# Optimization experiments

Hardware: AMD Instinct MI355X
Metric: run time of the kernel (lower is better)

Reference implementation:

```python
import jax, jax.numpy as jnp
import numpy as np

NHEADS = 16
KVHEADS = 4
HEAD_DIM = 128  # emb_kq_per_head == emb_v_per_head
ROPE_THETA = 10000.0


def _rotary(x, cos, sin):
    # x: [B, S, H, D]; half-split rotation
    x1, x2 = jnp.split(x, 2, axis=-1)
    rot = jnp.concatenate([-x2, x1], axis=-1)
    return x * cos + rot * sin


def setup_inputs() -> dict:
    key = jax.random.key(0)
    k1, k2, k3 = jax.random.split(key, 3)
    B, S, E = 2, 2048, 2048
    qkv_out = NHEADS * HEAD_DIM + 2 * KVHEADS * HEAD_DIM  # 3072
    return {
        "x": jax.random.normal(k1, (B, S, E), dtype=jnp.float32),
        "w_qkv": jax.random.normal(k2, (E, qkv_out), dtype=jnp.float32) * 0.02,
        "w_dense": jax.random.normal(k3, (NHEADS * HEAD_DIM, E), dtype=jnp.float32) * 0.02,
    }


def reference(x, w_qkv, w_dense):
    B, S, E = x.shape
    D = HEAD_DIM
    # fused QKV projection (use_bias=False), then split per FusedQKV.splits
    qkv = x @ w_qkv  # [B, S, 3072]
    q, k, v = jnp.split(qkv, [NHEADS * D, NHEADS * D + KVHEADS * D], axis=-1)
    q = q.reshape(B, S, NHEADS, D)
    k = k.reshape(B, S, KVHEADS, D)
    v = v.reshape(B, S, KVHEADS, D)

    # rotary position encoding, positions = arange(S)
    pos = jnp.arange(S, dtype=jnp.float32)
    inv_freq = 1.0 / (ROPE_THETA ** (jnp.arange(0, D, 2, dtype=jnp.float32) / D))
    ang = pos[:, None] * inv_freq[None, :]                 # [S, D/2]
    ang = jnp.concatenate([ang, ang], axis=-1)             # [S, D]
    cos = jnp.cos(ang)[None, :, None, :]                   # [1, S, 1, D]
    sin = jnp.sin(ang)[None, :, None, :]
    q = _rotary(q, cos, sin)
    k = _rotary(k, cos, sin)

    # GQA: expand kv heads to query heads
    rep = NHEADS // KVHEADS
    k = jnp.repeat(k, rep, axis=2)  # [B, S, NHEADS, D]
    v = jnp.repeat(v, rep, axis=2)

    scale = 1.0 / jnp.sqrt(jnp.asarray(D, dtype=x.dtype))
    scores = jnp.einsum("bqhd,bkhd->bhqk", q, k) * scale   # [B, H, S, S]
    causal = jnp.tril(jnp.ones((S, S), dtype=bool))
    scores = jnp.where(causal[None, None], scores, jnp.finfo(scores.dtype).min)
    probs = jax.nn.softmax(scores, axis=-1)
    attn = jnp.einsum("bhqk,bkhd->bqhd", probs, v)         # [B, S, H, D]
    attn = attn.reshape(B, S, NHEADS * D)
    return attn @ w_dense                                  # [B, S, E]
```

## Files before the change

### kernel.cpp

```cpp
#include <hip/hip_runtime.h>
#include <type_traits>


typedef __attribute__((ext_vector_type(8))) short short8;
typedef __attribute__((ext_vector_type(4))) float floatx4;
typedef __attribute__((ext_vector_type(4))) unsigned short ushort4v;

constexpr int NH    = 16;
constexpr int NKV   = 4;
constexpr int HD    = 128;
constexpr int SEQ   = 2048;
constexpr int EMB   = 2048;
constexpr int NBATCH = 2;
constexpr int MROWS = NBATCH * SEQ;
constexpr int NQKV  = (NH + 2 * NKV) * HD;

__device__ __forceinline__ unsigned short f2b(float f) {
  union { float f; unsigned u; } v; v.f = f;
  unsigned u = v.u + 0x7FFFu + ((v.u >> 16) & 1u);
  return (unsigned short)(u >> 16);
}
__device__ __forceinline__ float b2f(unsigned short h) {
  union { unsigned u; float f; } v; v.u = (unsigned)h << 16;
  return v.f;
}

__device__ __forceinline__ void gload_lds16(const unsigned short* g,
                                            unsigned short* lds) {
  __builtin_amdgcn_global_load_lds(
      (const __attribute__((address_space(1))) unsigned int*)g,
      (__attribute__((address_space(3))) unsigned int*)lds, 16, 0, 0);
}

__global__ void cvt_f32_bf16(const float* __restrict__ in,
                             unsigned short* __restrict__ out, int n) {
  int i = (blockIdx.x * 256 + threadIdx.x) * 4;
  if (i + 3 < n) {
    floatx4 v = *(const floatx4*)(in + i);
    ushort4v o = { f2b(v[0]), f2b(v[1]), f2b(v[2]), f2b(v[3]) };
    *(ushort4v*)(out + i) = o;
  }
}

__global__ void transpose_cvt_dual(const float* __restrict__ wqkv,
                                   unsigned short* __restrict__ oqkv,
                                   const float* __restrict__ wd,
                                   unsigned short* __restrict__ od) {
  const int z = blockIdx.z;
  const float* in = z ? wd : wqkv;
  unsigned short* out = z ? od : oqkv;
  const int R = EMB;
  const int C = z ? EMB : NQKV;
  int c0 = blockIdx.x * 32, r0 = blockIdx.y * 32;
  if (c0 >= C) return;
  __shared__ float t[32][33];
  int tx = threadIdx.x & 31, ty = threadIdx.x >> 5;
#pragma unroll
  for (int i = 0; i < 32; i += 8)
    t[ty + i][tx] = in[(long)(r0 + ty + i) * C + (c0 + tx)];
  __syncthreads();
#pragma unroll
  for (int i = 0; i < 32; i += 8)
    out[(long)(c0 + ty + i) * R + (r0 + tx)] = f2b(t[tx][ty + i]);
}

__global__ void rope_kernel(unsigned short* __restrict__ Qb,
                            unsigned short* __restrict__ Kb, float qscale) {
  int idx = blockIdx.x * 256 + threadIdx.x;
  int i = idx & 63;
  int s = (idx >> 6) & (SEQ - 1);
  int bh = idx >> 17;
  unsigned short* p;
  float scale;
  if (bh < NBATCH * NH) { p = Qb + ((long)bh * SEQ + s) * HD; scale = qscale; }
  else { p = Kb + ((long)(bh - NBATCH * NH) * SEQ + s) * HD; scale = 1.0f; }
  float e = -(float)i * (2.0f * 13.287712379549449f / 128.0f);
  float ang = (float)s * exp2f(e);
  float sn, c;
  sincosf(ang, &sn, &c);
  float x1 = b2f(p[i]), x2 = b2f(p[i + 64]);
  p[i]      = f2b((x1 * c - x2 * sn) * scale);
  p[i + 64] = f2b((x2 * c + x1 * sn) * scale);
}

constexpr int BM = 128, BN = 128, BK = 64;

template <int MODE>
__global__ __launch_bounds__(256, 3) void gemm_bt(
    const unsigned short* __restrict__ A,
    const unsigned short* __restrict__ BT,
    int Mdim, int Ndim, int Kdim,
    float* __restrict__ outF,
    unsigned short* __restrict__ Qb,
    unsigned short* __restrict__ Kb,
    unsigned short* __restrict__ Vt) {
  __shared__ __align__(16) unsigned short smem[BM * BK + BN * BK];
  unsigned short (*As)[BK] = (unsigned short (*)[BK])smem;
  unsigned short (*Bs)[BK] = (unsigned short (*)[BK])(smem + BM * BK);
  const int tid = threadIdx.x;
  const int bm = blockIdx.y * BM;
  const int bn = blockIdx.x * BN;
  const int wave = tid >> 6, lane = tid & 63;
  const int l = lane & 15, q = lane >> 4;
  const int l7 = l & 7;
  const int wm = (wave >> 1) * 64, wn = (wave & 1) * 64;

  floatx4 acc[4][4] = {};

  const int srow = lane >> 3;
  const int scol = ((lane & 7) ^ srow) * 8;
  const unsigned short* Arow = A + (long)bm * Kdim;
  const unsigned short* Brow = BT + (long)bn * Kdim;

  for (int k0 = 0; k0 < Kdim; k0 += BK) {
#pragma unroll
    for (int i = 0; i < 4; ++i) {
      const int r0 = wave * 32 + i * 8;
      gload_lds16(Arow + (long)(r0 + srow) * Kdim + k0 + scol, &As[r0][0]);
      gload_lds16(Brow + (long)(r0 + srow) * Kdim + k0 + scol, &Bs[r0][0]);
    }
    __syncthreads();
#pragma unroll
    for (int kk = 0; kk < 2; ++kk) {
      short8 af[4], bfr[4];
#pragma unroll
      for (int mi = 0; mi < 4; ++mi)
        af[mi] = *(const short8*)&As[wm + mi * 16 + l][((kk * 4 + q) ^ l7) * 8];
#pragma unroll
      for (int ni = 0; ni < 4; ++ni)
        bfr[ni] = *(const short8*)&Bs[wn + ni * 16 + l][((kk * 4 + q) ^ l7) * 8];
#pragma unroll
      for (int mi = 0; mi < 4; ++mi)
#pragma unroll
        for (int ni = 0; ni < 4; ++ni)
          acc[mi][ni] = __builtin_amdgcn_mfma_f32_16x16x32_bf16(
              af[mi], bfr[ni], acc[mi][ni], 0, 0, 0);
    }
    __syncthreads();
  }

  if constexpr (MODE == 1) {
#pragma unroll
    for (int mi = 0; mi < 4; ++mi) {
      const int rowbase = bm + wm + mi * 16 + q * 4;
#pragma unroll
      for (int ni = 0; ni < 4; ++ni) {
        const int col = bn + wn + ni * 16 + l;
#pragma unroll
        for (int r = 0; r < 4; ++r)
          outF[(long)(rowbase + r) * Ndim + col] = acc[mi][ni][r];
      }
    }
  } else if (bn >= (NH + NKV) * HD) {
    const int hh = (bn - (NH + NKV) * HD) >> 7;
#pragma unroll
    for (int mi = 0; mi < 4; ++mi) {
      const int m0 = bm + wm + mi * 16 + q * 4;
      const int bb = m0 >> 11, s = m0 & (SEQ - 1);
      unsigned short* vtb = Vt + ((long)(bb * NKV + hh)) * HD * SEQ;
#pragma unroll
      for (int ni = 0; ni < 4; ++ni) {
        const int d = wn + ni * 16 + l;
        ushort4v pv = { f2b(acc[mi][ni][0]), f2b(acc[mi][ni][1]),
                        f2b(acc[mi][ni][2]), f2b(acc[mi][ni][3]) };
        *(ushort4v*)(vtb + (long)d * SEQ + s) = pv;
      }
    }
  } else {
    unsigned short (*Ct)[128] = (unsigned short (*)[128])smem;
#pragma unroll
    for (int mi = 0; mi < 4; ++mi)
#pragma unroll
      for (int ni = 0; ni < 4; ++ni)
#pragma unroll
        for (int r = 0; r < 4; ++r) {
          const int row = wm + mi * 16 + q * 4 + r;
          const int col = wn + ni * 16 + l;
          const int cs = ((((col >> 3) ^ row) & 7) | (col & 64 ? 8 : 0)) * 8 + (col & 7);
          Ct[row][cs] = f2b(acc[mi][ni][r]);
        }
    __syncthreads();
    const int row = tid >> 1, g = tid & 1;
    const int m = bm + row, bb = m >> 11, s = m & (SEQ - 1);
    unsigned short* dst;
    if (bn < NH * HD)
      dst = Qb + (((long)(bb * NH + (bn >> 7))) * SEQ + s) * HD;
    else
      dst = Kb + (((long)(bb * NKV + ((bn - NH * HD) >> 7))) * SEQ + s) * HD;
#pragma unroll
    for (int i = 0; i < 8; ++i) {
      const int blk = (g * 8) + (i ^ (row & 7));
      *(short8*)(dst + g * 64 + i * 8) = *(const short8*)&Ct[row][blk * 8];
    }
  }
}

__global__ __launch_bounds__(256, 2) void attn_kernel(
    const unsigned short* __restrict__ Q,
    const unsigned short* __restrict__ K,
    const unsigned short* __restrict__ VT,
    unsigned short* __restrict__ attn) {
  const int pair = blockIdx.x, h = blockIdx.y, b = blockIdx.z;
  const int kvh = h >> 2;
  const int tid = threadIdx.x;
  const int wave = tid >> 6, lane = tid & 63;
  const int l = lane & 15, q = lane >> 4;
  const int l7 = l & 7;
  const int wq = wave * 16;

  const unsigned short* Kh = K + ((long)(b * NKV + kvh)) * SEQ * HD;
  const unsigned short* VTh = VT + ((long)(b * NKV + kvh)) * HD * SEQ;

  __shared__ __align__(16) unsigned short Ks[2][64 * 128];
  __shared__ __align__(16) unsigned short VTs[2][128 * 64];
  __shared__ __align__(16) unsigned short Ps[64][72];

  int koff[4], voff[4];
  {
    const int k_rl = lane >> 4, k_bp = lane & 15;
    const int v_rl = lane >> 3, v_bp = lane & 7;
#pragma unroll
    for (int j = 0; j < 4; ++j) {
      const int rk = (wave * 4 + j) * 4 + k_rl;
      koff[j] = rk * HD + (k_bp ^ (rk & 15)) * 8;
      const int rv = (wave * 4 + j) * 8 + v_rl;
      voff[j] = rv * SEQ + (v_bp ^ (rv & 7)) * 8;
    }
  }

  short8 onesf;
#pragma unroll
  for (int i = 0; i < 8; ++i) onesf[i] = (short)0x3F80;

  auto stage = [&](int c, int buf) {
    const unsigned short* kc = Kh + c * (64 * HD);
    const unsigned short* vc = VTh + c * 64;
#pragma unroll
    for (int j = 0; j < 4; ++j)
      gload_lds16(kc + koff[j], &Ks[buf][(wave * 4 + j) * 4 * 128]);
#pragma unroll
    for (int j = 0; j < 4; ++j)
      gload_lds16(vc + voff[j], &VTs[buf][(wave * 4 + j) * 8 * 64]);
  };

  auto chunk_body = [&](auto masked, int cur, int kv0, int qt,
                        short8* qf, floatx4* o) {
    constexpr bool MASKED = decltype(masked)::value;
    floatx4 sf[4] = {};
#pragma unroll
    for (int kk = 0; kk < 4; ++kk) {
      short8 kf[4];
#pragma unroll
      for (int ni = 0; ni < 4; ++ni) {
        const int row = ni * 16 + l;
        kf[ni] = *(const short8*)&Ks[cur][row * 128 + (((kk * 4 + q) ^ l) * 8)];
      }
#pragma unroll
      for (int ni = 0; ni < 4; ++ni)
        sf[ni] = __builtin_amdgcn_mfma_f32_16x16x32_bf16(
            qf[kk], kf[ni], sf[ni], 0, 0, 0);
    }
#pragma unroll
    for (int r = 0; r < 4; ++r) {
      if constexpr (MASKED) {
        const int qrow = qt * 64 + wq + q * 4 + r;
#pragma unroll
        for (int ni = 0; ni < 4; ++ni)
          if (kv0 + ni * 16 + l > qrow) sf[ni][r] = -3e38f;
      }
#pragma unroll
      for (int ni = 0; ni < 4; ++ni)
        Ps[wq + q * 4 + r][ni * 16 + l] = f2b(exp2f(sf[ni][r]));
    }
#pragma unroll
    for (int kvk = 0; kvk < 2; ++kvk) {
      short8 pf = *(const short8*)&Ps[wq + l][kvk * 32 + q * 8];
#pragma unroll
      for (int di = 0; di < 8; ++di) {
        const int row = di * 16 + l;
        short8 vf = *(const short8*)&VTs[cur][row * 64 + (((kvk * 4 + q) ^ l7) * 8)];
        o[di] = __builtin_amdgcn_mfma_f32_16x16x32_bf16(pf, vf, o[di], 0, 0, 0);
      }
      o[8] = __builtin_amdgcn_mfma_f32_16x16x32_bf16(pf, onesf, o[8], 0, 0, 0);
    }
  };

#pragma unroll 1
  for (int half = 0; half < 2; ++half) {
    const int qt = half ? (31 - pair) : pair;
    const unsigned short* Qh = Q + (((long)(b * NH + h)) * SEQ + qt * 64) * HD;

    short8 qf[4];
#pragma unroll
    for (int kk = 0; kk < 4; ++kk)
      qf[kk] = *(const short8*)(Qh + (long)(wq + l) * HD + kk * 32 + q * 8);

    floatx4 o[9] = {};
    const int nchunk = qt + 1;

    stage(0, 0);
    __syncthreads();

    int c = 0;
#pragma unroll 1
    for (; c < nchunk - 1; ++c) {
      stage(c + 1, (c & 1) ^ 1);
      chunk_body(std::false_type{}, c & 1, c * 64, qt, qf, o);
      __syncthreads();
    }
    chunk_body(std::true_type{}, c & 1, c * 64, qt, qf, o);
    __syncthreads();

    unsigned short (*Ob)[136] = (unsigned short (*)[136])&Ks[0][0];
#pragma unroll
    for (int r = 0; r < 4; ++r) {
      const float inv = 1.0f / o[8][r];
#pragma unroll
      for (int di = 0; di < 8; ++di)
        Ob[wq + q * 4 + r][di * 16 + l] = f2b(o[di][r] * inv);
    }
    __syncthreads();
    {
      const int row = tid >> 2, cg = (tid & 3) * 32;
      const int s = qt * 64 + row;
      unsigned short* dst = attn + ((long)(b * SEQ + s)) * (NH * HD) + h * HD + cg;
#pragma unroll
      for (int j = 0; j < 4; ++j)
        *(short8*)(dst + j * 8) = *(const short8*)&Ob[row][cg + j * 8];
    }
    __syncthreads();
  }
}

extern "C" void kernel_launch(void* const* d_in, const int* in_sizes, int n_in,
                              void* d_out, int out_size, void* d_ws, size_t ws_size,
                              hipStream_t stream) {
  const float* x       = (const float*)d_in[0];
  const float* w_qkv   = (const float*)d_in[1];
  const float* w_dense = (const float*)d_in[2];
  float* out = (float*)d_out;

  char* ws = (char*)d_ws;
  const size_t MB = 1024 * 1024;
  unsigned short* xb    = (unsigned short*)(ws);
  unsigned short* wqkvT = (unsigned short*)(ws + 16 * MB);
  unsigned short* wdT   = (unsigned short*)(ws + 28 * MB);
  unsigned short* Qb    = (unsigned short*)(ws + 36 * MB);
  unsigned short* Kb    = (unsigned short*)(ws + 52 * MB);
  unsigned short* VTb   = (unsigned short*)(ws + 56 * MB);
  unsigned short* attn  = xb;

  const float qscale = 0.08838834764831845f * 1.4426950408889634f;

  cvt_f32_bf16<<<(MROWS * EMB) / (256 * 4), 256, 0, stream>>>(x, xb, MROWS * EMB);
  transpose_cvt_dual<<<dim3(NQKV / 32, EMB / 32, 2), 256, 0, stream>>>(
      w_qkv, wqkvT, w_dense, wdT);

  gemm_bt<0><<<dim3(NQKV / BN, MROWS / BM), 256, 0, stream>>>(
      xb, wqkvT, MROWS, NQKV, EMB, nullptr, Qb, Kb, VTb);

  rope_kernel<<<(NBATCH * (NH + NKV) * SEQ * 64) / 256, 256, 0, stream>>>(Qb, Kb, qscale);

  attn_kernel<<<dim3(16, NH, NBATCH), 256, 0, stream>>>(Qb, Kb, VTb, attn);

  gemm_bt<1><<<dim3(EMB / BN, MROWS / BM), 256, 0, stream>>>(
      attn, wdT, MROWS, EMB, NH * HD, out, nullptr, nullptr, nullptr);
}
```

Measured before the change: 284.1 us.

## Give each attention block a 128-row query tile and reuse K/V fragments

New measurement: 301.8 us. 6.2% more time.

```diff
diff --git a/kernel.cpp b/kernel.cpp
--- a/kernel.cpp
+++ b/kernel.cpp
@@ -200,20 +200,21 @@
     const unsigned short* __restrict__ K,
     const unsigned short* __restrict__ VT,
     unsigned short* __restrict__ attn) {
-  const int pair = blockIdx.x, h = blockIdx.y, b = blockIdx.z;
+  const int h = blockIdx.y, b = blockIdx.z;
+  const int t = b ? (15 - (int)blockIdx.x) : (int)blockIdx.x;
   const int kvh = h >> 2;
   const int tid = threadIdx.x;
   const int wave = tid >> 6, lane = tid & 63;
   const int l = lane & 15, q = lane >> 4;
   const int l7 = l & 7;
-  const int wq = wave * 16;
-
-  const unsigned short* Kh = K + ((long)(b * NKV + kvh)) * SEQ * HD;
+  const int wq = wave * 32;
+
+  const unsigned short* Kh  = K  + ((long)(b * NKV + kvh)) * SEQ * HD;
   const unsigned short* VTh = VT + ((long)(b * NKV + kvh)) * HD * SEQ;
 
   __shared__ __align__(16) unsigned short Ks[2][64 * 128];
   __shared__ __align__(16) unsigned short VTs[2][128 * 64];
-  __shared__ __align__(16) unsigned short Ps[64][72];
+  __shared__ __align__(16) unsigned short Ps[128 * 64];
 
   int koff[4], voff[4];
   {
@@ -243,92 +244,107 @@
       gload_lds16(vc + voff[j], &VTs[buf][(wave * 4 + j) * 8 * 64]);
   };
 
-  auto chunk_body = [&](auto masked, int cur, int kv0, int qt,
-                        short8* qf, floatx4* o) {
+  const unsigned short* Qh = Q + (((long)(b * NH + h)) * SEQ + t * 128) * HD;
+  short8 qf[2][4];
+#pragma unroll
+  for (int mh = 0; mh < 2; ++mh)
+#pragma unroll
+    for (int kk = 0; kk < 4; ++kk)
+      qf[mh][kk] = *(const short8*)(Qh + (long)(wq + mh * 16 + l) * HD + kk * 32 + q * 8);
+
+  floatx4 o[2][9] = {};
+
+  auto chunk_body = [&](auto masked, int cur, int kv0) {
     constexpr bool MASKED = decltype(masked)::value;
-    floatx4 sf[4] = {};
+    floatx4 sf[2][4] = {};
 #pragma unroll
     for (int kk = 0; kk < 4; ++kk) {
       short8 kf[4];
 #pragma unroll
+      for (int ni = 0; ni < 4; ++ni)
+        kf[ni] = *(const short8*)&Ks[cur][(ni * 16 + l) * 128 + (((kk * 4 + q) ^ l) * 8)];
+#pragma unroll
+      for (int mh = 0; mh < 2; ++mh)
+#pragma unroll
+        for (int ni = 0; ni < 4; ++ni)
+          sf[mh][ni] = __builtin_amdgcn_mfma_f32_16x16x32_bf16(
+              kf[ni], qf[mh][kk], sf[mh][ni], 0, 0, 0);
+    }
+#pragma unroll
+    for (int mh = 0; mh < 2; ++mh) {
+      const int prow = wq + mh * 16 + l;
+      const int qrow = t * 128 + prow;
+#pragma unroll
       for (int ni = 0; ni < 4; ++ni) {
-        const int row = ni * 16 + l;
-        kf[ni] = *(const short8*)&Ks[cur][row * 128 + (((kk * 4 + q) ^ l) * 8)];
+        if constexpr (MASKED) {
+#pragma unroll
+          for (int r = 0; r < 4; ++r)
+            if (kv0 + ni * 16 + q * 4 + r > qrow) sf[mh][ni][r] = -3e38f;
+        }
+        float e0 = exp2f(sf[mh][ni][0]);
+        float e1 = exp2f(sf[mh][ni][1]);
+        float e2 = exp2f(sf[mh][ni][2]);
+        float e3 = exp2f(sf[mh][ni][3]);
+        unsigned u0, u1;
+        asm("v_cvt_pk_bf16_f32 %0, %1, %2" : "=v"(u0) : "v"(e0), "v"(e1));
+        asm("v_cvt_pk_bf16_f32 %0, %1, %2" : "=v"(u1) : "v"(e2), "v"(e3));
+        const int base = prow * 64 + (((ni * 2 + (q >> 1)) ^ l7) * 8) + (q & 1) * 4;
+        *(unsigned*)&Ps[base] = u0;
+        *(unsigned*)&Ps[base + 2] = u1;
       }
-#pragma unroll
-      for (int ni = 0; ni < 4; ++ni)
-        sf[ni] = __builtin_amdgcn_mfma_f32_16x16x32_bf16(
-            qf[kk], kf[ni], sf[ni], 0, 0, 0);
-    }
+    }
+#pragma unroll
+    for (int kvk = 0; kvk < 2; ++kvk) {
+      const int pb = ((kvk * 4 + q) ^ l7) * 8;
+      short8 pf0 = *(const short8*)&Ps[(wq + l) * 64 + pb];
+      short8 pf1 = *(const short8*)&Ps[(wq + 16 + l) * 64 + pb];
+#pragma unroll
+      for (int di = 0; di < 8; ++di) {
+        short8 vf = *(const short8*)&VTs[cur][(di * 16 + l) * 64 + pb];
+        o[0][di] = __builtin_amdgcn_mfma_f32_16x16x32_bf16(pf0, vf, o[0][di], 0, 0, 0);
+        o[1][di] = __builtin_amdgcn_mfma_f32_16x16x32_bf16(pf1, vf, o[1][di], 0, 0, 0);
+      }
+      o[0][8] = __builtin_amdgcn_mfma_f32_16x16x32_bf16(pf0, onesf, o[0][8], 0, 0, 0);
+      o[1][8] = __builtin_amdgcn_mfma_f32_16x16x32_bf16(pf1, onesf, o[1][8], 0, 0, 0);
+    }
+  };
+
+  const int nc = 2 * t + 2;
+  stage(0, 0);
+  __syncthreads();
+
+  int c = 0;
+#pragma unroll 1
+  for (; c < nc - 2; ++c) {
+    stage(c + 1, (c & 1) ^ 1);
+    chunk_body(std::false_type{}, c & 1, c * 64);
+    __syncthreads();
+  }
+  stage(c + 1, (c & 1) ^ 1);
+  chunk_body(std::true_type{}, c & 1, c * 64);
+  __syncthreads();
+  ++c;
+  chunk_body(std::true_type{}, c & 1, c * 64);
+  __syncthreads();
+
+  unsigned short (*Ob)[136] = (unsigned short (*)[136])&Ks[0][0];
+#pragma unroll
+  for (int mh = 0; mh < 2; ++mh)
 #pragma unroll
     for (int r = 0; r < 4; ++r) {
-      if constexpr (MASKED) {
-        const int qrow = qt * 64 + wq + q * 4 + r;
-#pragma unroll
-        for (int ni = 0; ni < 4; ++ni)
-          if (kv0 + ni * 16 + l > qrow) sf[ni][r] = -3e38f;
-      }
-#pragma unroll
-      for (int ni = 0; ni < 4; ++ni)
-        Ps[wq + q * 4 + r][ni * 16 + l] = f2b(exp2f(sf[ni][r]));
-    }
-#pragma unroll
-    for (int kvk = 0; kvk < 2; ++kvk) {
-      short8 pf = *(const short8*)&Ps[wq + l][kvk * 32 + q * 8];
-#pragma unroll
-      for (int di = 0; di < 8; ++di) {
-        const int row = di * 16 + l;
-        short8 vf = *(const short8*)&VTs[cur][row * 64 + (((kvk * 4 + q) ^ l7) * 8)];
-        o[di] = __builtin_amdgcn_mfma_f32_16x16x32_bf16(pf, vf, o[di], 0, 0, 0);
-      }
-      o[8] = __builtin_amdgcn_mfma_f32_16x16x32_bf16(pf, onesf, o[8], 0, 0, 0);
-    }
-  };
-
-#pragma unroll 1
-  for (int half = 0; half < 2; ++half) {
-    const int qt = half ? (31 - pair) : pair;
-    const unsigned short* Qh = Q + (((long)(b * NH + h)) * SEQ + qt * 64) * HD;
-
-    short8 qf[4];
-#pragma unroll
-    for (int kk = 0; kk < 4; ++kk)
-      qf[kk] = *(const short8*)(Qh + (long)(wq + l) * HD + kk * 32 + q * 8);
-
-    floatx4 o[9] = {};
-    const int nchunk = qt + 1;
-
-    stage(0, 0);
-    __syncthreads();
-
-    int c = 0;
-#pragma unroll 1
-    for (; c < nchunk - 1; ++c) {
-      stage(c + 1, (c & 1) ^ 1);
-      chunk_body(std::false_type{}, c & 1, c * 64, qt, qf, o);
-      __syncthreads();
-    }
-    chunk_body(std::true_type{}, c & 1, c * 64, qt, qf, o);
-    __syncthreads();
-
-    unsigned short (*Ob)[136] = (unsigned short (*)[136])&Ks[0][0];
-#pragma unroll
-    for (int r = 0; r < 4; ++r) {
-      const float inv = 1.0f / o[8][r];
+      const float inv = 1.0f / o[mh][8][r];
 #pragma unroll
       for (int di = 0; di < 8; ++di)
-        Ob[wq + q * 4 + r][di * 16 + l] = f2b(o[di][r] * inv);
-    }
-    __syncthreads();
-    {
-      const int row = tid >> 2, cg = (tid & 3) * 32;
-      const int s = qt * 64 + row;
-      unsigned short* dst = attn + ((long)(b * SEQ + s)) * (NH * HD) + h * HD + cg;
-#pragma unroll
-      for (int j = 0; j < 4; ++j)
-        *(short8*)(dst + j * 8) = *(const short8*)&Ob[row][cg + j * 8];
-    }
-    __syncthreads();
+        Ob[wq + mh * 16 + q * 4 + r][di * 16 + l] = f2b(o[mh][di][r] * inv);
+    }
+  __syncthreads();
+  {
+    const int row = tid >> 1, g = (tid & 1) * 64;
+    const int s = t * 128 + row;
+    unsigned short* dst = attn + ((long)(b * SEQ + s)) * (NH * HD) + h * HD + g;
+#pragma unroll
+    for (int j = 0; j < 8; ++j)
+      *(short8*)(dst + j * 8) = *(const short8*)&Ob[row][g + j * 8];
   }
 }
 
```
